# Kernel optimization log

Measured on AMD Instinct MI355X. Metric: run time of the kernel, lower is better.

Reference implementation:

```python
import jax, jax.numpy as jnp
import numpy as np

M1 = M2 = M3 = 8  # retained modes per spatial dim


def get_3d_clifford_kernel(w, g):
    # w: (8, O, I, 2m1, 2m2, 2m3); returns (8O, 8I, 2m1, 2m2, 2m3)
    g0, g1, g2 = g[0], g[1], g[2]
    k0 = jnp.concatenate([w[0], w[1] * g0, w[2] * g1, w[3] * g2, -w[4] * g0 * g1, -w[5] * g0 * g2, -w[6] * g1 * g2, -w[7] * g0 * g1 * g2], axis=1)
    k1 = jnp.concatenate([w[1], w[0], -w[4] * g1, -w[5] * g2, w[2] * g1, w[3] * g2, -w[7] * g1 * g2, -w[6] * g1 * g2], axis=1)
    k2 = jnp.concatenate([w[2], w[4] * g0, w[0], -w[6] * g2, -w[1] * g0, w[7] * g0 * g2, w[3] * g2, w[5] * g0 * g2], axis=1)
    k3 = jnp.concatenate([w[3], w[5] * g0, w[6] * g1, w[0], -w[7] * g0 * g1, -w[1] * g0, -w[2] * g1, -w[4] * g0 * g1], axis=1)
    k4 = jnp.concatenate([w[4], w[2], -w[1], g2 * w[7], w[0], -w[6] * g2, w[5] * g2, w[3] * g2], axis=1)
    k5 = jnp.concatenate([w[5], w[3], -w[7] * g1, -w[1], w[6] * g1, w[0], -w[4] * g1, -w[2] * g1], axis=1)
    k6 = jnp.concatenate([w[6], w[7] * g0, w[3], -w[2], -w[5] * g0, w[4] * g0, w[0], w[1] * g0], axis=1)
    k7 = jnp.concatenate([w[7], w[6], -w[5], w[4], w[3], -w[2], w[1], w[0]], axis=1)
    return jnp.concatenate([k0, k1, k2, k3, k4, k5, k6, k7], axis=0)


def setup_inputs() -> dict:
    key = jax.random.key(0)
    k1, k2 = jax.random.split(key)
    B, D, H, W, Cin, Cout = 4, 48, 48, 48, 24, 24
    x = jax.random.normal(k1, (B, D, H, W, Cin, 8), dtype=jnp.float32)
    scale = 1.0 / (Cin * Cout)
    weights = scale * jax.random.uniform(k2, (8, Cout, Cin, 2 * M1, 2 * M2, 2 * M3), dtype=jnp.float32)
    return {"x": x, "weights": weights}


def reference(x, weights):
    B, D, H, W, Cin, _ = x.shape
    Cout = weights.shape[1]
    g = jnp.ones(3, dtype=x.dtype)  # metric (1, 1, 1)
    # complex-dual packing of the 8 blades
    d1 = x[..., 0] + 1j * x[..., 7]
    d2 = x[..., 1] + 1j * x[..., 6]
    d3 = x[..., 2] + 1j * x[..., 5]
    d4 = x[..., 3] + 1j * x[..., 4]
    f1 = jnp.fft.fftn(d1, axes=(1, 2, 3))
    f2 = jnp.fft.fftn(d2, axes=(1, 2, 3))
    f3 = jnp.fft.fftn(d3, axes=(1, 2, 3))
    f4 = jnp.fft.fftn(d4, axes=(1, 2, 3))
    bchw = lambda t: t.transpose(0, 4, 1, 2, 3)
    # (B, 8*Cin, D, H, W) real tensor of blade spectra
    mv_ft = jnp.concatenate([bchw(f1.real), bchw(f2.real), bchw(f3.real), bchw(f4.real),
                             bchw(f4.imag), bchw(f3.imag), bchw(f2.imag), bchw(f1.imag)], axis=1)
    # gather the 8 low/high-frequency octant corners -> (B, 8Cin, 2m1, 2m2, 2m3)
    i1 = jnp.concatenate([jnp.arange(M1), jnp.arange(D - M1, D)])
    i2 = jnp.concatenate([jnp.arange(M2), jnp.arange(H - M2, H)])
    i3 = jnp.concatenate([jnp.arange(M3), jnp.arange(W - M3, W)])
    input_mul = mv_ft[:, :, i1[:, None, None], i2[None, :, None], i3[None, None, :]]
    kernel = get_3d_clifford_kernel(weights, g)  # (8Cout, 8Cin, 2m1, 2m2, 2m3)
    output_mul = jnp.einsum("bixyz,oixyz->boxyz", input_mul, kernel)
    # scatter back to full spectrum
    out_ft = jnp.zeros((B, 8 * Cout, D, H, W), dtype=mv_ft.dtype)
    out_ft = out_ft.at[:, :, i1[:, None, None], i2[None, :, None], i3[None, None, :]].set(output_mul)
    out_ft = out_ft.reshape(B, 8, Cout, D, H, W).transpose(0, 2, 3, 4, 5, 1)  # (B, Cout, D, H, W, 8)
    o1 = out_ft[..., 0] + 1j * out_ft[..., 7]
    o2 = out_ft[..., 1] + 1j * out_ft[..., 6]
    o3 = out_ft[..., 2] + 1j * out_ft[..., 5]
    o4 = out_ft[..., 3] + 1j * out_ft[..., 4]
    g1_ = jnp.fft.ifftn(o1, axes=(2, 3, 4))
    g2_ = jnp.fft.ifftn(o2, axes=(2, 3, 4))
    g3_ = jnp.fft.ifftn(o3, axes=(2, 3, 4))
    g4_ = jnp.fft.ifftn(o4, axes=(2, 3, 4))
    output = jnp.stack([g1_.real, g2_.real, g3_.real, g4_.real,
                        g4_.imag, g3_.imag, g2_.imag, g1_.imag], axis=-1)  # (B, Cout, D, H, W, 8)
    return output.transpose(0, 2, 3, 4, 1, 5)  # (B, D, H, W, Cout, 8)
```

## Files before the change

### kernel.cpp

```cpp
#include <hip/hip_runtime.h>
#include <math.h>


#define C866 0.8660254037844386f

constexpr float FC0[8] = {1.0f, 0.99144486137885f, 0.96592582628907f, 0.92387953251129f,
                          0.86602540378444f, 0.79335334029124f, 0.70710678118655f, 0.60876142900872f};
constexpr float FS0[8] = {0.0f, 0.13052619222005f, 0.25881904510252f, 0.38268343236509f,
                          0.5f, 0.60876142900872f, 0.70710678118655f, 0.79335334029124f};
constexpr float FC1[8] = {0.5f, 0.60876142900872f, 0.70710678118655f, 0.79335334029124f,
                          0.86602540378444f, 0.92387953251129f, 0.96592582628907f, 0.99144486137885f};
constexpr float FS1[8] = {-0.86602540378444f, -0.79335334029124f, -0.70710678118655f, -0.60876142900872f,
                          -0.5f, -0.38268343236509f, -0.25881904510252f, -0.13052619222005f};

__device__ __forceinline__ uint32_t c2h(float2 z) {
  union { _Float16 h[2]; uint32_t u; } v;
  v.h[0] = (_Float16)z.x; v.h[1] = (_Float16)z.y;
  return v.u;
}
__device__ __forceinline__ float2 h2c(uint32_t u) {
  union { uint32_t u; _Float16 h[2]; } v;
  v.u = u;
  return make_float2((float)v.h[0], (float)v.h[1]);
}

__device__ __forceinline__ float2 cmul(float2 a, float2 b) {
  return make_float2(fmaf(a.x, b.x, -(a.y * b.y)), fmaf(a.x, b.y, a.y * b.x));
}
__device__ __forceinline__ void cfma(float2& acc, float2 a, float2 t) {
  acc.x = fmaf(a.x, t.x, acc.x); acc.x = fmaf(-a.y, t.y, acc.x);
  acc.y = fmaf(a.x, t.y, acc.y); acc.y = fmaf(a.y, t.x, acc.y);
}

struct FwdState {
  float2 acc[8], t[8], stp[8];
  float2 R1, R2;
};

__device__ __forceinline__ void fwd_init(FwdState& st, int half) {
#pragma unroll
  for (int r = 0; r < 8; ++r) {
    st.acc[r] = make_float2(0.f, 0.f);
    st.t[r] = make_float2(1.f, 0.f);
    st.stp[r] = make_float2(half ? FC1[r] : FC0[r],
                            half ? -FS1[r] : -FS0[r]);
  }
  st.R1 = half ? make_float2(-0.5f, -C866) : make_float2(1.f, 0.f);
  st.R2 = half ? make_float2(-0.5f,  C866) : make_float2(1.f, 0.f);
}

__device__ __forceinline__ void fwd_stepf(FwdState& st, float2 z0, float2 z1, float2 z2) {
  z1 = cmul(z1, st.R1);
  z2 = cmul(z2, st.R2);
  const float sx = z1.x + z2.x, sy = z1.y + z2.y;
  const float dx = z1.x - z2.x, dy = z1.y - z2.y;
  const float2 y0 = make_float2(z0.x + sx, z0.y + sy);
  const float tx = fmaf(-0.5f, sx, z0.x), ty = fmaf(-0.5f, sy, z0.y);
  const float ex = C866 * dx, ey = C866 * dy;
  const float2 y1 = make_float2(tx + ey, ty - ex);
  const float2 y2 = make_float2(tx - ey, ty + ex);
#pragma unroll
  for (int r = 0; r < 8; ++r) {
    const float2 yy = (r % 3 == 0) ? y0 : ((r % 3 == 1) ? y1 : y2);
    cfma(st.acc[r], yy, st.t[r]);
    st.t[r] = cmul(st.t[r], st.stp[r]);
  }
}

struct InvState {
  float2 zr[16], t[16];
};

__device__ __forceinline__ void inv_init(InvState& st) {
#pragma unroll
  for (int m = 0; m < 16; ++m) st.t[m] = make_float2(1.f, 0.f);
}

__device__ __forceinline__ void inv_stepf(InvState& st, float2& o0, float2& o1, float2& o2) {
  constexpr int JG[16] = {0,1,2,0,1,2,0,1, 1,2,0,1,2,0,1,2};
  float2 u0 = make_float2(0.f, 0.f), u1 = u0, u2 = u0;
#pragma unroll
  for (int m = 0; m < 16; ++m) {
    float2& uu = (JG[m] == 0) ? u0 : ((JG[m] == 1) ? u1 : u2);
    cfma(uu, st.zr[m], st.t[m]);
    const float2 stp = (m < 8) ? make_float2(FC0[m], FS0[m])
                               : make_float2(FC1[m - 8], FS1[m - 8]);
    st.t[m] = cmul(st.t[m], stp);
  }
  const float sx = u1.x + u2.x, sy = u1.y + u2.y;
  const float dx = u1.x - u2.x, dy = u1.y - u2.y;
  o0 = make_float2(u0.x + sx, u0.y + sy);
  const float tx = fmaf(-0.5f, sx, u0.x), ty = fmaf(-0.5f, sy, u0.y);
  const float ex = C866 * dx, ey = C866 * dy;
  o1 = make_float2(tx - ey, ty + ex);
  o2 = make_float2(tx + ey, ty - ex);
}

__global__ __launch_bounds__(192) void k_fwd_w(const float* __restrict__ x,
                                               uint32_t* __restrict__ A) {
  __shared__ __align__(16) uint32_t xs[48 * 96];
  {
    const float* xp = x + (size_t)blockIdx.x * 9216;
    for (int idx = threadIdx.x; idx < 1152; idx += 192) {
      const int w = idx / 24, ci = idx % 24;
      const float4 u = *(const float4*)(xp + w * 192 + ci * 8);
      const float4 v = *(const float4*)(xp + w * 192 + ci * 8 + 4);
      uint4 d;
      d.x = c2h(make_float2(u.x, v.w));
      d.y = c2h(make_float2(u.y, v.z));
      d.z = c2h(make_float2(u.z, v.y));
      d.w = c2h(make_float2(u.w, v.x));
      *(uint4*)(&xs[w * 96 + ci * 4]) = d;
    }
  }
  __syncthreads();

  const int q = threadIdx.x % 96, half = threadIdx.x / 96;
  FwdState st;
  fwd_init(st, half);
#pragma unroll 4
  for (int j = 0; j < 16; ++j) {
    const float2 z0 = h2c(xs[j * 96 + q]);
    const float2 z1 = h2c(xs[(j + 16) * 96 + q]);
    const float2 z2 = h2c(xs[(j + 32) * 96 + q]);
    fwd_stepf(st, z0, z1, z2);
  }
  uint32_t* Ap = A + (size_t)blockIdx.x * 1536 + q;
#pragma unroll
  for (int r = 0; r < 8; ++r) Ap[(half * 8 + r) * 96] = c2h(st.acc[r]);
}

__global__ __launch_bounds__(192) void k_fwd_h(const uint32_t* __restrict__ A,
                                               uint32_t* __restrict__ Bv) {
  const int k3 = blockIdx.x & 15, bd = blockIdx.x >> 4;
  const int q = threadIdx.x % 96, half = threadIdx.x / 96;
  const uint32_t* Ap = A + ((size_t)bd * 768 + k3) * 96 + q;
  FwdState st;
  fwd_init(st, half);
#pragma unroll 4
  for (int j = 0; j < 16; ++j) {
    const float2 z0 = h2c(Ap[(size_t)j * 1536]);
    const float2 z1 = h2c(Ap[(size_t)(j + 16) * 1536]);
    const float2 z2 = h2c(Ap[(size_t)(j + 32) * 1536]);
    fwd_stepf(st, z0, z1, z2);
  }
  uint32_t* Bp = Bv + ((size_t)bd * 256 + k3) * 96 + q;
#pragma unroll
  for (int r = 0; r < 8; ++r) Bp[(size_t)(half * 8 + r) * 1536] = c2h(st.acc[r]);
}

__global__ __launch_bounds__(192) void k_fwd_d(const uint32_t* __restrict__ Bv,
                                               uint32_t* __restrict__ Cv) {
  const int k23 = blockIdx.x & 255, b = blockIdx.x >> 8;
  const int q = threadIdx.x % 96, half = threadIdx.x / 96;
  const uint32_t* Bp = Bv + ((size_t)b * 12288 + k23) * 96 + q;
  FwdState st;
  fwd_init(st, half);
#pragma unroll 4
  for (int j = 0; j < 16; ++j) {
    const float2 z0 = h2c(Bp[(size_t)j * 24576]);
    const float2 z1 = h2c(Bp[(size_t)(j + 16) * 24576]);
    const float2 z2 = h2c(Bp[(size_t)(j + 32) * 24576]);
    fwd_stepf(st, z0, z1, z2);
  }
  uint32_t* Cp = Cv + ((size_t)b * 4096 + k23) * 96 + q;
#pragma unroll
  for (int r = 0; r < 8; ++r) Cp[(size_t)(half * 8 + r) * 24576] = c2h(st.acc[r]);
}

__global__ __launch_bounds__(256) void k_einsum(const uint32_t* __restrict__ Cv,
                                                const float* __restrict__ wgt,
                                                uint32_t* __restrict__ OMz) {
  const int mode = blockIdx.x * 64 + (threadIdx.x & 63);
  const int co = blockIdx.y * 4 + (threadIdx.x >> 6);

  constexpr int WIDX[8][8] = {
      {0, 1, 2, 3, 4, 5, 6, 7}, {1, 0, 4, 5, 2, 3, 7, 6},
      {2, 4, 0, 6, 1, 7, 3, 5}, {3, 5, 6, 0, 7, 1, 2, 4},
      {4, 2, 1, 7, 0, 6, 5, 3}, {5, 3, 7, 1, 6, 0, 4, 2},
      {6, 7, 3, 2, 5, 4, 0, 1}, {7, 6, 5, 4, 3, 2, 1, 0}};
  constexpr int SGN[8][8] = {
      {1, 1, 1, 1, -1, -1, -1, -1}, {1, 1, -1, -1, 1, 1, -1, -1},
      {1, 1, 1, -1, -1, 1, 1, 1},   {1, 1, 1, 1, -1, -1, -1, -1},
      {1, 1, -1, 1, 1, -1, 1, 1},   {1, 1, -1, -1, 1, 1, -1, -1},
      {1, 1, 1, -1, -1, 1, 1, 1},   {1, 1, -1, 1, 1, -1, 1, 1}};

  float acc[8][4];
#pragma unroll
  for (int bo = 0; bo < 8; ++bo)
#pragma unroll
    for (int b = 0; b < 4; ++b) acc[bo][b] = 0.f;

  for (int ci = 0; ci < 24; ++ci) {
    float w8[8];
#pragma unroll
    for (int k = 0; k < 8; ++k)
      w8[k] = wgt[(size_t)((k * 24 + co) * 24 + ci) * 4096 + mode];
#pragma unroll
    for (int b = 0; b < 4; ++b) {
      const uint4 U = *(const uint4*)(Cv + ((size_t)(b * 4096 + mode) * 96 + ci * 4));
      const float2 z0 = h2c(U.x), z1 = h2c(U.y), z2 = h2c(U.z), z3 = h2c(U.w);
      const float inv[8] = {z0.x, z1.x, z2.x, z3.x, z3.y, z2.y, z1.y, z0.y};
#pragma unroll
      for (int bo = 0; bo < 8; ++bo) {
#pragma unroll
        for (int bi = 0; bi < 8; ++bi) {
          const float wv = w8[WIDX[bo][bi]];
          if (SGN[bo][bi] > 0)
            acc[bo][b] = fmaf(wv, inv[bi], acc[bo][b]);
          else
            acc[bo][b] = fmaf(wv, -inv[bi], acc[bo][b]);
        }
      }
    }
  }
#pragma unroll
  for (int b = 0; b < 4; ++b) {
    uint4 P;
    P.x = c2h(make_float2(acc[0][b], acc[7][b]));
    P.y = c2h(make_float2(acc[1][b], acc[6][b]));
    P.z = c2h(make_float2(acc[2][b], acc[5][b]));
    P.w = c2h(make_float2(acc[3][b], acc[4][b]));
    *(uint4*)(OMz + ((size_t)(b * 4096 + mode) * 96 + co * 4)) = P;
  }
}

__global__ __launch_bounds__(192) void k_inv_d(const uint32_t* __restrict__ OMz,
                                               uint32_t* __restrict__ IS1) {
  const int col = blockIdx.x * 2 + threadIdx.x / 96;
  const int q = threadIdx.x % 96;
  const int k23 = col & 255, b = col >> 8;
  InvState st;
#pragma unroll
  for (int m = 0; m < 16; ++m)
    st.zr[m] = h2c(OMz[((size_t)b * 4096 + m * 256 + k23) * 96 + q]);
  inv_init(st);
  uint32_t* Op = IS1 + ((size_t)b * 12288 + k23) * 96 + q;
#pragma unroll 2
  for (int j = 0; j < 16; ++j) {
    float2 o0, o1, o2;
    inv_stepf(st, o0, o1, o2);
    Op[(size_t)j * 24576] = c2h(o0);
    Op[(size_t)(j + 16) * 24576] = c2h(o1);
    Op[(size_t)(j + 32) * 24576] = c2h(o2);
  }
}

__global__ __launch_bounds__(192) void k_inv_h(const uint32_t* __restrict__ IS1,
                                               uint32_t* __restrict__ IS2) {
  const int col = blockIdx.x * 2 + threadIdx.x / 96;
  const int q = threadIdx.x % 96;
  const int m3 = col & 15, bd = col >> 4;
  InvState st;
#pragma unroll
  for (int m = 0; m < 16; ++m)
    st.zr[m] = h2c(IS1[((size_t)bd * 256 + m * 16 + m3) * 96 + q]);
  inv_init(st);
  uint32_t* Op = IS2 + ((size_t)bd * 768 + m3) * 96 + q;
#pragma unroll 2
  for (int j = 0; j < 16; ++j) {
    float2 o0, o1, o2;
    inv_stepf(st, o0, o1, o2);
    Op[(size_t)j * 1536] = c2h(o0);
    Op[(size_t)(j + 16) * 1536] = c2h(o1);
    Op[(size_t)(j + 32) * 1536] = c2h(o2);
  }
}

__global__ __launch_bounds__(192) void k_inv_w(const uint32_t* __restrict__ IS2,
                                               float* __restrict__ out) {
  const int blk = blockIdx.x * 2 + threadIdx.x / 96;
  const int q = threadIdx.x % 96;
  const int co = q >> 2, c = q & 3;
  const float norm = 1.0f / 110592.0f;
  InvState st;
#pragma unroll
  for (int m = 0; m < 16; ++m) {
    float2 z = h2c(IS2[((size_t)blk * 16 + m) * 96 + q]);
    st.zr[m] = make_float2(z.x * norm, z.y * norm);
  }
  inv_init(st);
  float* ob = out + (size_t)blk * 9216 + co * 8;
#pragma unroll 2
  for (int j = 0; j < 16; ++j) {
    float2 o0, o1, o2;
    inv_stepf(st, o0, o1, o2);
    float* p0 = ob + (size_t)j * 192;
    float* p1 = ob + (size_t)(j + 16) * 192;
    float* p2 = ob + (size_t)(j + 32) * 192;
    p0[c] = o0.x; p0[7 - c] = o0.y;
    p1[c] = o1.x; p1[7 - c] = o1.y;
    p2[c] = o2.x; p2[7 - c] = o2.y;
  }
}

extern "C" void kernel_launch(void* const* d_in, const int* in_sizes, int n_in,
                              void* d_out, int out_size, void* d_ws, size_t ws_size,
                              hipStream_t stream) {
  (void)in_sizes; (void)n_in; (void)out_size; (void)ws_size;
  const float* x = (const float*)d_in[0];
  const float* wgt = (const float*)d_in[1];
  float* out = (float*)d_out;

  char* ob = (char*)d_out;
  uint32_t* A   = (uint32_t*)(ob + 0);
  uint32_t* Bv  = (uint32_t*)(ob + 56623104);
  uint32_t* Cv  = (uint32_t*)(ob + 75497472);
  uint32_t* OMz = (uint32_t*)(ob + 81788928);
  uint32_t* IS1 = (uint32_t*)(ob + 0);
  uint32_t* IS2 = (uint32_t*)d_ws;

  k_fwd_w<<<9216, 192, 0, stream>>>(x, A);
  k_fwd_h<<<3072, 192, 0, stream>>>(A, Bv);
  k_fwd_d<<<1024, 192, 0, stream>>>(Bv, Cv);
  k_einsum<<<dim3(64, 6), 256, 0, stream>>>(Cv, wgt, OMz);
  k_inv_d<<<512, 192, 0, stream>>>(OMz, IS1);
  k_inv_h<<<1536, 192, 0, stream>>>(IS1, IS2);
  k_inv_w<<<4608, 192, 0, stream>>>(IS2, out);
}
```

Before: 314.2 us.

## Split einsum over input channels, split inverse-D over output rows, drop LDS staging

The einsum is split into two halves over input channels, each writing its own partial buffer, and the inverse-D pass sums the two partials on load. Inverse-D also gets a second grid dimension that splits the 16 output steps, with twiddles started at the right phase from a 48-entry table. This puts more blocks on the device for the low-occupancy stages. The forward-W kernel now reads input directly from global memory instead of staging it as half precision in shared memory, and the final output uses nontemporal stores. In exchange, inverse-D does its partial-sum loads twice, the partial buffer needs extra space, and the direct loads in forward-W are strided.

```diff
diff --git a/kernel.cpp b/kernel.cpp
--- a/kernel.cpp
+++ b/kernel.cpp
@@ -12,6 +12,30 @@
                           0.86602540378444f, 0.92387953251129f, 0.96592582628907f, 0.99144486137885f};
 constexpr float FS1[8] = {-0.86602540378444f, -0.79335334029124f, -0.70710678118655f, -0.60876142900872f,
                           -0.5f, -0.38268343236509f, -0.25881904510252f, -0.13052619222005f};
+
+constexpr float CS48[48] = {
+  1.0f, 0.99144486137885f, 0.96592582628907f, 0.92387953251129f, 0.86602540378444f,
+  0.79335334029124f, 0.70710678118655f, 0.60876142900872f, 0.5f, 0.38268343236509f,
+  0.25881904510252f, 0.13052619222005f, 0.0f, -0.13052619222005f, -0.25881904510252f,
+  -0.38268343236509f, -0.5f, -0.60876142900872f, -0.70710678118655f, -0.79335334029124f,
+  -0.86602540378444f, -0.92387953251129f, -0.96592582628907f, -0.99144486137885f, -1.0f,
+  -0.99144486137885f, -0.96592582628907f, -0.92387953251129f, -0.86602540378444f,
+  -0.79335334029124f, -0.70710678118655f, -0.60876142900872f, -0.5f, -0.38268343236509f,
+  -0.25881904510252f, -0.13052619222005f, 0.0f, 0.13052619222005f, 0.25881904510252f,
+  0.38268343236509f, 0.5f, 0.60876142900872f, 0.70710678118655f, 0.79335334029124f,
+  0.86602540378444f, 0.92387953251129f, 0.96592582628907f, 0.99144486137885f};
+constexpr float SN48[48] = {
+  0.0f, 0.13052619222005f, 0.25881904510252f, 0.38268343236509f, 0.5f,
+  0.60876142900872f, 0.70710678118655f, 0.79335334029124f, 0.86602540378444f,
+  0.92387953251129f, 0.96592582628907f, 0.99144486137885f, 1.0f, 0.99144486137885f,
+  0.96592582628907f, 0.92387953251129f, 0.86602540378444f, 0.79335334029124f,
+  0.70710678118655f, 0.60876142900872f, 0.5f, 0.38268343236509f, 0.25881904510252f,
+  0.13052619222005f, 0.0f, -0.13052619222005f, -0.25881904510252f, -0.38268343236509f,
+  -0.5f, -0.60876142900872f, -0.70710678118655f, -0.79335334029124f, -0.86602540378444f,
+  -0.92387953251129f, -0.96592582628907f, -0.99144486137885f, -1.0f, -0.99144486137885f,
+  -0.96592582628907f, -0.92387953251129f, -0.86602540378444f, -0.79335334029124f,
+  -0.70710678118655f, -0.60876142900872f, -0.5f, -0.38268343236509f, -0.25881904510252f,
+  -0.13052619222005f};
 
 __device__ __forceinline__ uint32_t c2h(float2 z) {
   union { _Float16 h[2]; uint32_t u; } v;
@@ -71,9 +95,13 @@
   float2 zr[16], t[16];
 };
 
-__device__ __forceinline__ void inv_init(InvState& st) {
-#pragma unroll
-  for (int m = 0; m < 16; ++m) st.t[m] = make_float2(1.f, 0.f);
+__device__ __forceinline__ void inv_init(InvState& st, int j0) {
+#pragma unroll
+  for (int m = 0; m < 16; ++m) {
+    const int f = (m < 8) ? m : (m + 32);
+    const int ph = (f * j0) % 48;
+    st.t[m] = make_float2(CS48[ph], SN48[ph]);
+  }
 }
 
 __device__ __forceinline__ void inv_stepf(InvState& st, float2& o0, float2& o1, float2& o2) {
@@ -98,31 +126,18 @@
 
 __global__ __launch_bounds__(192) void k_fwd_w(const float* __restrict__ x,
                                                uint32_t* __restrict__ A) {
-  __shared__ __align__(16) uint32_t xs[48 * 96];
-  {
-    const float* xp = x + (size_t)blockIdx.x * 9216;
-    for (int idx = threadIdx.x; idx < 1152; idx += 192) {
-      const int w = idx / 24, ci = idx % 24;
-      const float4 u = *(const float4*)(xp + w * 192 + ci * 8);
-      const float4 v = *(const float4*)(xp + w * 192 + ci * 8 + 4);
-      uint4 d;
-      d.x = c2h(make_float2(u.x, v.w));
-      d.y = c2h(make_float2(u.y, v.z));
-      d.z = c2h(make_float2(u.z, v.y));
-      d.w = c2h(make_float2(u.w, v.x));
-      *(uint4*)(&xs[w * 96 + ci * 4]) = d;
-    }
-  }
-  __syncthreads();
-
   const int q = threadIdx.x % 96, half = threadIdx.x / 96;
+  const int ci = q >> 2, c = q & 3;
+  const float* xp = x + (size_t)blockIdx.x * 9216 + ci * 8;
+  const int reo = c, imo = 7 - c;
+
   FwdState st;
   fwd_init(st, half);
 #pragma unroll 4
   for (int j = 0; j < 16; ++j) {
-    const float2 z0 = h2c(xs[j * 96 + q]);
-    const float2 z1 = h2c(xs[(j + 16) * 96 + q]);
-    const float2 z2 = h2c(xs[(j + 32) * 96 + q]);
+    const float2 z0 = make_float2(xp[j * 192 + reo], xp[j * 192 + imo]);
+    const float2 z1 = make_float2(xp[(j + 16) * 192 + reo], xp[(j + 16) * 192 + imo]);
+    const float2 z2 = make_float2(xp[(j + 32) * 192 + reo], xp[(j + 32) * 192 + imo]);
     fwd_stepf(st, z0, z1, z2);
   }
   uint32_t* Ap = A + (size_t)blockIdx.x * 1536 + q;
@@ -173,6 +188,7 @@
                                                 uint32_t* __restrict__ OMz) {
   const int mode = blockIdx.x * 64 + (threadIdx.x & 63);
   const int co = blockIdx.y * 4 + (threadIdx.x >> 6);
+  const int cih = blockIdx.z;
 
   constexpr int WIDX[8][8] = {
       {0, 1, 2, 3, 4, 5, 6, 7}, {1, 0, 4, 5, 2, 3, 7, 6},
@@ -191,7 +207,9 @@
 #pragma unroll
     for (int b = 0; b < 4; ++b) acc[bo][b] = 0.f;
 
-  for (int ci = 0; ci < 24; ++ci) {
+#pragma unroll 2
+  for (int cc = 0; cc < 12; ++cc) {
+    const int ci = cih * 12 + cc;
     float w8[8];
 #pragma unroll
     for (int k = 0; k < 8; ++k)
@@ -214,6 +232,7 @@
       }
     }
   }
+  uint32_t* OMp = OMz + (size_t)cih * 1572864;
 #pragma unroll
   for (int b = 0; b < 4; ++b) {
     uint4 P;
@@ -221,7 +240,7 @@
     P.y = c2h(make_float2(acc[1][b], acc[6][b]));
     P.z = c2h(make_float2(acc[2][b], acc[5][b]));
     P.w = c2h(make_float2(acc[3][b], acc[4][b]));
-    *(uint4*)(OMz + ((size_t)(b * 4096 + mode) * 96 + co * 4)) = P;
+    *(uint4*)(OMp + ((size_t)(b * 4096 + mode) * 96 + co * 4)) = P;
   }
 }
 
@@ -230,14 +249,20 @@
   const int col = blockIdx.x * 2 + threadIdx.x / 96;
   const int q = threadIdx.x % 96;
   const int k23 = col & 255, b = col >> 8;
+  const int j0 = blockIdx.y * 8;
   InvState st;
 #pragma unroll
-  for (int m = 0; m < 16; ++m)
-    st.zr[m] = h2c(OMz[((size_t)b * 4096 + m * 256 + k23) * 96 + q]);
-  inv_init(st);
+  for (int m = 0; m < 16; ++m) {
+    const size_t idx = ((size_t)b * 4096 + m * 256 + k23) * 96 + q;
+    const float2 pa = h2c(OMz[idx]);
+    const float2 pb = h2c(OMz[idx + 1572864]);
+    st.zr[m] = make_float2(pa.x + pb.x, pa.y + pb.y);
+  }
+  inv_init(st, j0);
   uint32_t* Op = IS1 + ((size_t)b * 12288 + k23) * 96 + q;
 #pragma unroll 2
-  for (int j = 0; j < 16; ++j) {
+  for (int jj = 0; jj < 8; ++jj) {
+    const int j = j0 + jj;
     float2 o0, o1, o2;
     inv_stepf(st, o0, o1, o2);
     Op[(size_t)j * 24576] = c2h(o0);
@@ -255,7 +280,7 @@
 #pragma unroll
   for (int m = 0; m < 16; ++m)
     st.zr[m] = h2c(IS1[((size_t)bd * 256 + m * 16 + m3) * 96 + q]);
-  inv_init(st);
+  inv_init(st, 0);
   uint32_t* Op = IS2 + ((size_t)bd * 768 + m3) * 96 + q;
 #pragma unroll 2
   for (int j = 0; j < 16; ++j) {
@@ -279,7 +304,7 @@
     float2 z = h2c(IS2[((size_t)blk * 16 + m) * 96 + q]);
     st.zr[m] = make_float2(z.x * norm, z.y * norm);
   }
-  inv_init(st);
+  inv_init(st, 0);
   float* ob = out + (size_t)blk * 9216 + co * 8;
 #pragma unroll 2
   for (int j = 0; j < 16; ++j) {
@@ -288,9 +313,12 @@
     float* p0 = ob + (size_t)j * 192;
     float* p1 = ob + (size_t)(j + 16) * 192;
     float* p2 = ob + (size_t)(j + 32) * 192;
-    p0[c] = o0.x; p0[7 - c] = o0.y;
-    p1[c] = o1.x; p1[7 - c] = o1.y;
-    p2[c] = o2.x; p2[7 - c] = o2.y;
+    __builtin_nontemporal_store(o0.x, p0 + c);
+    __builtin_nontemporal_store(o0.y, p0 + 7 - c);
+    __builtin_nontemporal_store(o1.x, p1 + c);
+    __builtin_nontemporal_store(o1.y, p1 + 7 - c);
+    __builtin_nontemporal_store(o2.x, p2 + c);
+    __builtin_nontemporal_store(o2.y, p2 + 7 - c);
   }
 }
 
@@ -313,8 +341,8 @@
   k_fwd_w<<<9216, 192, 0, stream>>>(x, A);
   k_fwd_h<<<3072, 192, 0, stream>>>(A, Bv);
   k_fwd_d<<<1024, 192, 0, stream>>>(Bv, Cv);
-  k_einsum<<<dim3(64, 6), 256, 0, stream>>>(Cv, wgt, OMz);
-  k_inv_d<<<512, 192, 0, stream>>>(OMz, IS1);
+  k_einsum<<<dim3(64, 6, 2), 256, 0, stream>>>(Cv, wgt, OMz);
+  k_inv_d<<<dim3(512, 2), 192, 0, stream>>>(OMz, IS1);
   k_inv_h<<<1536, 192, 0, stream>>>(IS1, IS2);
   k_inv_w<<<4608, 192, 0, stream>>>(IS2, out);
 }
```

New measurement: 324.8 us. 1.03x slower.
